# Performance work log

Measured on AMD Instinct MI355X. Metric: run time of the kernel, lower is better.

Reference implementation:

```python
import jax, jax.numpy as jnp
import numpy as np

NUM_HEADS = 8

def setup_inputs() -> dict:
    key = jax.random.key(0)
    k1, k2, k3, k4 = jax.random.split(key, 4)
    B, N, C = 2, 4096, 768
    x = jax.random.normal(k1, (B, N, C), dtype=jnp.float32)
    w_qkv = jax.random.normal(k2, (C, 3 * C), dtype=jnp.float32) * (C ** -0.5)
    w_proj = jax.random.normal(k3, (C, C), dtype=jnp.float32) * (C ** -0.5)
    b_proj = jax.random.normal(k4, (C,), dtype=jnp.float32) * 0.02
    return {"x": x, "w_qkv": w_qkv, "w_proj": w_proj, "b_proj": b_proj}

def reference(x, w_qkv, w_proj, b_proj):
    B, N, C = x.shape
    H = NUM_HEADS
    Dh = C // H
    scale = Dh ** -0.5
    # qkv: [B, N, 3C] -> [B, N, 3, H, Dh] -> [3, B, H, N, Dh]
    qkv = (x @ w_qkv).reshape(B, N, 3, H, Dh).transpose(2, 0, 3, 1, 4)
    q, k, v = qkv[0], qkv[1], qkv[2]
    attn = jnp.einsum('bhqd,bhkd->bhqk', q, k) * scale  # [B,H,N,N]
    attn = jax.nn.softmax(attn, axis=-1)
    out = jnp.einsum('bhqk,bhkd->bhqd', attn, v)        # [B,H,N,Dh]
    out = out.transpose(0, 2, 1, 3).reshape(B, N, C)
    return out @ w_proj + b_proj
```

## Files before the change

### kernel.cpp

```cpp
#include <hip/hip_runtime.h>
#include <hip/hip_bf16.h>

typedef __attribute__((ext_vector_type(8))) short short8;
typedef __attribute__((ext_vector_type(4))) short short4v;
typedef __attribute__((ext_vector_type(4))) float f32x4;
typedef __attribute__((ext_vector_type(16))) float f32x16;

#define MFMA16(a,b,c) __builtin_amdgcn_mfma_f32_16x16x32_bf16(a,b,c,0,0,0)
#define MFMA32(a,b,c) __builtin_amdgcn_mfma_f32_32x32x16_bf16(a,b,c,0,0,0)

__device__ __forceinline__ unsigned short f2b_rne(float f){
  union { float f; unsigned int u; } v; v.f = f;
  unsigned int u = v.u;
  return (unsigned short)((u + 0x7FFFu + ((u >> 16) & 1u)) >> 16);
}

__device__ __forceinline__ f32x16 zero16(){
  f32x16 z;
  #pragma unroll
  for (int i = 0; i < 16; ++i) z[i] = 0.f;
  return z;
}

__global__ __launch_bounds__(256) void k_cvt(const float* __restrict__ in,
                                             unsigned short* __restrict__ out, int n8){
  int i = blockIdx.x * 256 + threadIdx.x;
  if (i >= n8) return;
  const float4* p = (const float4*)in + (size_t)i * 2;
  float4 a = p[0], b = p[1];
  short8 o;
  o[0] = (short)f2b_rne(a.x); o[1] = (short)f2b_rne(a.y);
  o[2] = (short)f2b_rne(a.z); o[3] = (short)f2b_rne(a.w);
  o[4] = (short)f2b_rne(b.x); o[5] = (short)f2b_rne(b.y);
  o[6] = (short)f2b_rne(b.z); o[7] = (short)f2b_rne(b.w);
  *((short8*)out + i) = o;
}

__global__ void k_transpose_cvt(const float* __restrict__ in, unsigned short* __restrict__ out,
                                int R, int Cc){
  __shared__ unsigned short tile[32][33];
  int c0 = blockIdx.x * 32, r0 = blockIdx.y * 32;
  int tx = threadIdx.x, ty = threadIdx.y;
  #pragma unroll
  for (int i = 0; i < 32; i += 8)
    tile[ty + i][tx] = f2b_rne(in[(size_t)(r0 + ty + i) * Cc + c0 + tx]);
  __syncthreads();
  #pragma unroll
  for (int i = 0; i < 32; i += 8)
    out[(size_t)(c0 + ty + i) * R + r0 + tx] = tile[tx][ty + i];
}

__global__ __launch_bounds__(256) void k_gemm_qkv(
    const unsigned short* __restrict__ A,
    const unsigned short* __restrict__ Bt,
    unsigned short* __restrict__ qbuf,
    unsigned short* __restrict__ kbuf,
    unsigned short* __restrict__ vtb)
{
  __shared__ short As[128 * 40];
  __shared__ short Bs[128 * 40];
  int m0 = blockIdx.x * 128, n0 = blockIdx.y * 128;
  int t = threadIdx.x, l = t & 63, w = t >> 6;
  int lr = l & 15, lh = l >> 4;
  int wr = w >> 1, wc = w & 1;

  int row0 = t >> 2, cs0 = t & 3;
  int row1 = row0 + 64;
  const unsigned short* ga0 = A  + (size_t)(m0 + row0) * 768 + cs0 * 8;
  const unsigned short* ga1 = A  + (size_t)(m0 + row1) * 768 + cs0 * 8;
  const unsigned short* gb0 = Bt + (size_t)(n0 + row0) * 768 + cs0 * 8;
  const unsigned short* gb1 = Bt + (size_t)(n0 + row1) * 768 + cs0 * 8;
  short* la0 = As + row0 * 40 + cs0 * 8;
  short* la1 = As + row1 * 40 + cs0 * 8;
  short* lb0 = Bs + row0 * 40 + cs0 * 8;
  short* lb1 = Bs + row1 * 40 + cs0 * 8;

  f32x4 acc[4][4];
  f32x4 z4 = {0.f, 0.f, 0.f, 0.f};
  #pragma unroll
  for (int mf = 0; mf < 4; ++mf)
    #pragma unroll
    for (int nf = 0; nf < 4; ++nf) acc[mf][nf] = z4;

  short8 ra0 = *(const short8*)ga0;
  short8 ra1 = *(const short8*)ga1;
  short8 rb0 = *(const short8*)gb0;
  short8 rb1 = *(const short8*)gb1;

  for (int kt = 0; kt < 24; ++kt){
    __syncthreads();
    *(short8*)la0 = ra0; *(short8*)la1 = ra1;
    *(short8*)lb0 = rb0; *(short8*)lb1 = rb1;
    __syncthreads();
    if (kt < 23){
      ra0 = *(const short8*)(ga0 + (kt + 1) * 32);
      ra1 = *(const short8*)(ga1 + (kt + 1) * 32);
      rb0 = *(const short8*)(gb0 + (kt + 1) * 32);
      rb1 = *(const short8*)(gb1 + (kt + 1) * 32);
    }
    short8 af[4], bfm[4];
    #pragma unroll
    for (int mf = 0; mf < 4; ++mf)
      af[mf] = *(const short8*)(As + (wr * 64 + mf * 16 + lr) * 40 + lh * 8);
    #pragma unroll
    for (int nf = 0; nf < 4; ++nf)
      bfm[nf] = *(const short8*)(Bs + (wc * 64 + nf * 16 + lr) * 40 + lh * 8);
    #pragma unroll
    for (int mf = 0; mf < 4; ++mf)
      #pragma unroll
      for (int nf = 0; nf < 4; ++nf)
        acc[mf][nf] = MFMA16(af[mf], bfm[nf], acc[mf][nf]);
  }

  const float qscale = 0.10206207261596577f * 1.4426950408889634f;
  int three = n0 / 768;
  int b_ = m0 >> 12;
  int ntok0 = m0 & 4095;
  #pragma unroll
  for (int nf = 0; nf < 4; ++nf){
    int gcol = n0 + wc * 64 + nf * 16 + lr;
    int jj = gcol - three * 768;
    int h = jj / 96;
    int dh = jj - h * 96;
    #pragma unroll
    for (int mf = 0; mf < 4; ++mf){
      int ntok = ntok0 + wr * 64 + mf * 16 + lh * 4;
      if (three == 0){
        unsigned short* dst = qbuf + (size_t)(b_ * 8 + h) * 4096 * 96;
        #pragma unroll
        for (int r = 0; r < 4; ++r)
          dst[(size_t)(ntok + r) * 96 + dh] = f2b_rne(acc[mf][nf][r] * qscale);
      } else if (three == 1){
        unsigned short* dst = kbuf + (size_t)(b_ * 8 + h) * 4096 * 96;
        #pragma unroll
        for (int r = 0; r < 4; ++r)
          dst[(size_t)(ntok + r) * 96 + dh] = f2b_rne(acc[mf][nf][r]);
      } else {
        short4v sv;
        #pragma unroll
        for (int r = 0; r < 4; ++r) sv[r] = (short)f2b_rne(acc[mf][nf][r]);
        *(short4v*)(vtb + ((size_t)(b_ * 8 + h) * 96 + dh) * 4096 + ntok) = sv;
      }
    }
  }
}

__global__ __launch_bounds__(512) void k_attn2(
    const unsigned short* __restrict__ qb,
    const unsigned short* __restrict__ kb,
    const unsigned short* __restrict__ vtb,
    unsigned short* __restrict__ ao)
{
  __shared__ short lds[27136];
  const int bh = blockIdx.x;
  const int qt = blockIdx.y;
  const int tid = threadIdx.x;
  const int ln = tid & 63, wid = tid >> 6;
  const int qc = ln & 31, hi = ln >> 5;
  const int q0 = qt * 256 + wid * 32;

  const unsigned short* qbase = qb  + (size_t)bh * 4096 * 96;
  const unsigned short* kbase = kb  + (size_t)bh * 4096 * 96;
  const unsigned short* vbase = vtb + (size_t)bh * 96 * 4096;

  short8 qf[6];
  #pragma unroll
  for (int kw = 0; kw < 6; ++kw)
    qf[kw] = *(const short8*)(qbase + (size_t)(q0 + qc) * 96 + kw * 16 + hi * 8);

  const unsigned short* gp[3]; int gstep[3], loff[3], lstep[3];
  #pragma unroll
  for (int j = 0; j < 3; ++j){
    int c = tid + j * 512;
    if (c < 768){
      int r = c / 12, cl = c - r * 12;
      gp[j] = kbase + r * 96 + cl * 8; gstep[j] = 64 * 96;
      loff[j] = r * 104 + cl * 8;      lstep[j] = 6656;
    } else {
      int cv = c - 768; int r = cv >> 3, cl = cv & 7;
      gp[j] = vbase + (size_t)r * 4096 + cl * 8; gstep[j] = 64;
      loff[j] = 13312 + r * 72 + cl * 8;         lstep[j] = 6912;
    }
  }

  short8 rs[3];
  #pragma unroll
  for (int j = 0; j < 3; ++j){ rs[j] = *(const short8*)gp[j]; gp[j] += gstep[j]; }
  #pragma unroll
  for (int j = 0; j < 3; ++j) *(short8*)(lds + loff[j]) = rs[j];

  f32x16 oacc[3];
  #pragma unroll
  for (int dt = 0; dt < 3; ++dt) oacc[dt] = zero16();
  float m = -1e30f, lsum = 0.f;

  const int krd = qc * 104 + hi * 8;
  const int vrd = 13312 + qc * 72 + hi * 8;

#define CVTPK(d, lo_, hi_) asm("v_cvt_pk_bf16_f32 %0, %1, %2" : "=v"(d) : "v"(lo_), "v"(hi_))
#define PLSWAP(x_, y_)     asm("v_permlane32_swap_b32 %0, %1" : "+v"(x_), "+v"(y_))

  for (int kt = 0; kt < 64; ++kt){
    const int cur = kt & 1;
    __syncthreads();
    if (kt < 63){
      #pragma unroll
      for (int j = 0; j < 3; ++j){ rs[j] = *(const short8*)gp[j]; gp[j] += gstep[j]; }
    }
    const short* Kb = lds + cur * 6656 + krd;
    const short* Vb = lds + cur * 6912 + vrd;

    f32x16 s0 = zero16(), s1 = zero16();
    __builtin_amdgcn_s_setprio(1);
    #pragma unroll
    for (int kw = 0; kw < 6; ++kw){
      short8 kf = *(const short8*)(Kb + kw * 16);
      s0 = MFMA32(kf, qf[kw], s0);
    }
    #pragma unroll
    for (int kw = 0; kw < 6; ++kw){
      short8 kf = *(const short8*)(Kb + 32 * 104 + kw * 16);
      s1 = MFMA32(kf, qf[kw], s1);
    }
    __builtin_amdgcn_s_setprio(0);

    float tmax = s0[0];
    #pragma unroll
    for (int r = 1; r < 16; ++r) tmax = fmaxf(tmax, s0[r]);
    #pragma unroll
    for (int r = 0; r < 16; ++r) tmax = fmaxf(tmax, s1[r]);
    tmax = fmaxf(tmax, __shfl_xor(tmax, 32, 64));
    float mnew = fmaxf(m, tmax);
    float alpha = exp2f(m - mnew);
    m = mnew;
    float psum = 0.f;
    #pragma unroll
    for (int r = 0; r < 16; ++r){ float p = exp2f(s0[r] - m); s0[r] = p; psum += p; }
    #pragma unroll
    for (int r = 0; r < 16; ++r){ float p = exp2f(s1[r] - m); s1[r] = p; psum += p; }
    psum += __shfl_xor(psum, 32, 64);
    lsum = lsum * alpha + psum;
    #pragma unroll
    for (int dt = 0; dt < 3; ++dt)
      #pragma unroll
      for (int r = 0; r < 16; ++r) oacc[dt][r] *= alpha;

    short8 pa[4];
    {
      unsigned int a, b;
      union { unsigned int u[4]; short8 s; } pk;
      CVTPK(a, s0[0], s0[1]);  CVTPK(b, s0[4],  s0[5]);  PLSWAP(a, b); pk.u[0] = a; pk.u[2] = b;
      CVTPK(a, s0[2], s0[3]);  CVTPK(b, s0[6],  s0[7]);  PLSWAP(a, b); pk.u[1] = a; pk.u[3] = b;
      pa[0] = pk.s;
      CVTPK(a, s0[8], s0[9]);  CVTPK(b, s0[12], s0[13]); PLSWAP(a, b); pk.u[0] = a; pk.u[2] = b;
      CVTPK(a, s0[10], s0[11]); CVTPK(b, s0[14], s0[15]); PLSWAP(a, b); pk.u[1] = a; pk.u[3] = b;
      pa[1] = pk.s;
      CVTPK(a, s1[0], s1[1]);  CVTPK(b, s1[4],  s1[5]);  PLSWAP(a, b); pk.u[0] = a; pk.u[2] = b;
      CVTPK(a, s1[2], s1[3]);  CVTPK(b, s1[6],  s1[7]);  PLSWAP(a, b); pk.u[1] = a; pk.u[3] = b;
      pa[2] = pk.s;
      CVTPK(a, s1[8], s1[9]);  CVTPK(b, s1[12], s1[13]); PLSWAP(a, b); pk.u[0] = a; pk.u[2] = b;
      CVTPK(a, s1[10], s1[11]); CVTPK(b, s1[14], s1[15]); PLSWAP(a, b); pk.u[1] = a; pk.u[3] = b;
      pa[3] = pk.s;
    }

    __builtin_amdgcn_s_setprio(1);
    #pragma unroll
    for (int dt = 0; dt < 3; ++dt){
      #pragma unroll
      for (int w = 0; w < 4; ++w){
        short8 vf = *(const short8*)(Vb + dt * 32 * 72 + w * 16);
        oacc[dt] = MFMA32(vf, pa[w], oacc[dt]);
      }
    }
    __builtin_amdgcn_s_setprio(0);

    if (kt < 63){
      const int nb = cur ^ 1;
      #pragma unroll
      for (int j = 0; j < 3; ++j) *(short8*)(lds + loff[j] + nb * lstep[j]) = rs[j];
    }
  }

  float inv = 1.0f / lsum;
  int b_ = bh >> 3, h = bh & 7;
  unsigned short* orow = ao + (size_t)(b_ * 4096 + q0 + qc) * 768 + h * 96;
  #pragma unroll
  for (int dt = 0; dt < 3; ++dt)
    #pragma unroll
    for (int g = 0; g < 4; ++g){
      short4v sv;
      #pragma unroll
      for (int r = 0; r < 4; ++r) sv[r] = (short)f2b_rne(oacc[dt][g * 4 + r] * inv);
      *(short4v*)(orow + dt * 32 + g * 8 + hi * 4) = sv;
    }
#undef CVTPK
#undef PLSWAP
}

__global__ __launch_bounds__(256) void k_gemm_proj(
    const unsigned short* __restrict__ A,
    const unsigned short* __restrict__ Bt,
    const float* __restrict__ bias,
    float* __restrict__ out)
{
  __shared__ short As[128 * 40];
  __shared__ short Bs[128 * 40];
  int m0 = blockIdx.x * 128, n0 = blockIdx.y * 128;
  int t = threadIdx.x, l = t & 63, w = t >> 6;
  int lr = l & 15, lh = l >> 4;
  int wr = w >> 1, wc = w & 1;

  int row0 = t >> 2, cs0 = t & 3;
  int row1 = row0 + 64;
  const unsigned short* ga0 = A  + (size_t)(m0 + row0) * 768 + cs0 * 8;
  const unsigned short* ga1 = A  + (size_t)(m0 + row1) * 768 + cs0 * 8;
  const unsigned short* gb0 = Bt + (size_t)(n0 + row0) * 768 + cs0 * 8;
  const unsigned short* gb1 = Bt + (size_t)(n0 + row1) * 768 + cs0 * 8;
  short* la0 = As + row0 * 40 + cs0 * 8;
  short* la1 = As + row1 * 40 + cs0 * 8;
  short* lb0 = Bs + row0 * 40 + cs0 * 8;
  short* lb1 = Bs + row1 * 40 + cs0 * 8;

  f32x4 acc[4][4];
  f32x4 z4 = {0.f, 0.f, 0.f, 0.f};
  #pragma unroll
  for (int mf = 0; mf < 4; ++mf)
    #pragma unroll
    for (int nf = 0; nf < 4; ++nf) acc[mf][nf] = z4;

  short8 ra0 = *(const short8*)ga0;
  short8 ra1 = *(const short8*)ga1;
  short8 rb0 = *(const short8*)gb0;
  short8 rb1 = *(const short8*)gb1;

  for (int kt = 0; kt < 24; ++kt){
    __syncthreads();
    *(short8*)la0 = ra0; *(short8*)la1 = ra1;
    *(short8*)lb0 = rb0; *(short8*)lb1 = rb1;
    __syncthreads();
    if (kt < 23){
      ra0 = *(const short8*)(ga0 + (kt + 1) * 32);
      ra1 = *(const short8*)(ga1 + (kt + 1) * 32);
      rb0 = *(const short8*)(gb0 + (kt + 1) * 32);
      rb1 = *(const short8*)(gb1 + (kt + 1) * 32);
    }
    short8 af[4], bfm[4];
    #pragma unroll
    for (int mf = 0; mf < 4; ++mf)
      af[mf] = *(const short8*)(As + (wr * 64 + mf * 16 + lr) * 40 + lh * 8);
    #pragma unroll
    for (int nf = 0; nf < 4; ++nf)
      bfm[nf] = *(const short8*)(Bs + (wc * 64 + nf * 16 + lr) * 40 + lh * 8);
    #pragma unroll
    for (int mf = 0; mf < 4; ++mf)
      #pragma unroll
      for (int nf = 0; nf < 4; ++nf)
        acc[mf][nf] = MFMA16(af[mf], bfm[nf], acc[mf][nf]);
  }

  #pragma unroll
  for (int nf = 0; nf < 4; ++nf){
    int gcol = n0 + wc * 64 + nf * 16 + lr;
    float bb = bias[gcol];
    #pragma unroll
    for (int mf = 0; mf < 4; ++mf){
      int grow = m0 + wr * 64 + mf * 16 + lh * 4;
      #pragma unroll
      for (int r = 0; r < 4; ++r)
        out[(size_t)(grow + r) * 768 + gcol] = acc[mf][nf][r] + bb;
    }
  }
}

extern "C" void kernel_launch(void* const* d_in, const int* in_sizes, int n_in,
                              void* d_out, int out_size, void* d_ws, size_t ws_size,
                              hipStream_t stream) {
  const float* x      = (const float*)d_in[0];
  const float* w_qkv  = (const float*)d_in[1];
  const float* w_proj = (const float*)d_in[2];
  const float* b_proj = (const float*)d_in[3];
  float* out = (float*)d_out;
  char* ws = (char*)d_ws;

  unsigned short* xb     = (unsigned short*)(ws);
  unsigned short* wqkvt  = (unsigned short*)(ws + 12582912);
  unsigned short* wprojt = (unsigned short*)(ws + 16121856);
  unsigned short* qbuf   = (unsigned short*)(ws + 17301504);
  unsigned short* kbuf   = (unsigned short*)(ws + 29884416);
  unsigned short* vtb    = (unsigned short*)(ws + 42467328);
  unsigned short* aob    = xb;

  k_cvt<<<3072, 256, 0, stream>>>(x, xb, 786432);
  k_transpose_cvt<<<dim3(72, 24), dim3(32, 8), 0, stream>>>(w_qkv, wqkvt, 768, 2304);
  k_transpose_cvt<<<dim3(24, 24), dim3(32, 8), 0, stream>>>(w_proj, wprojt, 768, 768);
  k_gemm_qkv<<<dim3(64, 18), 256, 0, stream>>>(xb, wqkvt, qbuf, kbuf, vtb);
  k_attn2<<<dim3(16, 16), 512, 0, stream>>>(qbuf, kbuf, vtb, aob);
  k_gemm_proj<<<dim3(64, 6), 256, 0, stream>>>(aob, wprojt, b_proj, out);
}
```

Measured before the change: 229.5 us.

## Split KV range across two warp sets with 64-row queries per warp and lazy rescale

The attention kernel now has each warp handle 64 query rows (two 32-row groups), so every K/V fragment read from LDS feeds two MFMAs. The eight warps form two sets that process alternate 64-key tiles, and their partial softmax states are merged through LDS at the end. Online-softmax rescaling is skipped unless the running max grows by more than 8, and the global prefetch is placed between the two softmax passes. The cost is higher register pressure from doubled accumulators, a two-barrier single-buffer loop, and an LDS-based merge epilogue.

```diff
diff --git a/kernel.cpp b/kernel.cpp
--- a/kernel.cpp
+++ b/kernel.cpp
@@ -145,7 +145,7 @@
   }
 }
 
-__global__ __launch_bounds__(512) void k_attn2(
+__global__ __launch_bounds__(512) void k_attn3(
     const unsigned short* __restrict__ qb,
     const unsigned short* __restrict__ kb,
     const unsigned short* __restrict__ vtb,
@@ -157,144 +157,215 @@
   const int tid = threadIdx.x;
   const int ln = tid & 63, wid = tid >> 6;
   const int qc = ln & 31, hi = ln >> 5;
-  const int q0 = qt * 256 + wid * 32;
+  const int set = wid >> 2, qquad = wid & 3;
+  const int q0 = qt * 256 + qquad * 64;
 
   const unsigned short* qbase = qb  + (size_t)bh * 4096 * 96;
   const unsigned short* kbase = kb  + (size_t)bh * 4096 * 96;
   const unsigned short* vbase = vtb + (size_t)bh * 96 * 4096;
 
-  short8 qf[6];
-  #pragma unroll
-  for (int kw = 0; kw < 6; ++kw)
-    qf[kw] = *(const short8*)(qbase + (size_t)(q0 + qc) * 96 + kw * 16 + hi * 8);
-
-  const unsigned short* gp[3]; int gstep[3], loff[3], lstep[3];
-  #pragma unroll
-  for (int j = 0; j < 3; ++j){
+  short8 qf[2][6];
+  #pragma unroll
+  for (int g = 0; g < 2; ++g)
+    #pragma unroll
+    for (int kw = 0; kw < 6; ++kw)
+      qf[g][kw] = *(const short8*)(qbase + (size_t)(q0 + g * 32 + qc) * 96 + kw * 16 + hi * 8);
+
+  const unsigned short* gp[6]; int gstep[6], loff[6];
+  #pragma unroll
+  for (int j = 0; j < 6; ++j){
     int c = tid + j * 512;
-    if (c < 768){
-      int r = c / 12, cl = c - r * 12;
-      gp[j] = kbase + r * 96 + cl * 8; gstep[j] = 64 * 96;
-      loff[j] = r * 104 + cl * 8;      lstep[j] = 6656;
+    int s = (c >= 1536) ? 1 : 0;
+    int cc = c - s * 1536;
+    if (cc < 768){
+      int r = cc / 12, cl = cc - r * 12;
+      gp[j] = kbase + (size_t)(s * 64 + r) * 96 + cl * 8; gstep[j] = 12288;
+      loff[j] = s * 6656 + r * 104 + cl * 8;
     } else {
-      int cv = c - 768; int r = cv >> 3, cl = cv & 7;
-      gp[j] = vbase + (size_t)r * 4096 + cl * 8; gstep[j] = 64;
-      loff[j] = 13312 + r * 72 + cl * 8;         lstep[j] = 6912;
-    }
-  }
-
-  short8 rs[3];
-  #pragma unroll
-  for (int j = 0; j < 3; ++j){ rs[j] = *(const short8*)gp[j]; gp[j] += gstep[j]; }
-  #pragma unroll
-  for (int j = 0; j < 3; ++j) *(short8*)(lds + loff[j]) = rs[j];
-
-  f32x16 oacc[3];
-  #pragma unroll
-  for (int dt = 0; dt < 3; ++dt) oacc[dt] = zero16();
-  float m = -1e30f, lsum = 0.f;
-
-  const int krd = qc * 104 + hi * 8;
-  const int vrd = 13312 + qc * 72 + hi * 8;
+      int cv = cc - 768; int r = cv >> 3, cl = cv & 7;
+      gp[j] = vbase + (size_t)r * 4096 + s * 64 + cl * 8; gstep[j] = 128;
+      loff[j] = 13312 + s * 6912 + r * 72 + cl * 8;
+    }
+  }
+
+  short8 rs[6];
+  #pragma unroll
+  for (int j = 0; j < 6; ++j){ rs[j] = *(const short8*)gp[j]; gp[j] += gstep[j]; }
+  #pragma unroll
+  for (int j = 0; j < 6; ++j) *(short8*)(lds + loff[j]) = rs[j];
+
+  f32x16 oacc[2][3];
+  #pragma unroll
+  for (int g = 0; g < 2; ++g)
+    #pragma unroll
+    for (int dt = 0; dt < 3; ++dt) oacc[g][dt] = zero16();
+  float mr[2] = {-1e30f, -1e30f}, lr_[2] = {0.f, 0.f};
+
+  const short* Kb = lds + set * 6656 + qc * 104 + hi * 8;
+  const short* Vb = lds + 13312 + set * 6912 + qc * 72 + hi * 8;
 
 #define CVTPK(d, lo_, hi_) asm("v_cvt_pk_bf16_f32 %0, %1, %2" : "=v"(d) : "v"(lo_), "v"(hi_))
 #define PLSWAP(x_, y_)     asm("v_permlane32_swap_b32 %0, %1" : "+v"(x_), "+v"(y_))
 
-  for (int kt = 0; kt < 64; ++kt){
-    const int cur = kt & 1;
-    __syncthreads();
-    if (kt < 63){
-      #pragma unroll
-      for (int j = 0; j < 3; ++j){ rs[j] = *(const short8*)gp[j]; gp[j] += gstep[j]; }
-    }
-    const short* Kb = lds + cur * 6656 + krd;
-    const short* Vb = lds + cur * 6912 + vrd;
-
-    f32x16 s0 = zero16(), s1 = zero16();
+#define PA_BUILD(pa_, sA_, sB_)                                                          \
+  {                                                                                      \
+    unsigned int a_, b_;                                                                 \
+    union { unsigned int u[4]; short8 s; } pk_;                                          \
+    CVTPK(a_, sA_[0],  sA_[1]);  CVTPK(b_, sA_[4],  sA_[5]);  PLSWAP(a_, b_); pk_.u[0]=a_; pk_.u[2]=b_; \
+    CVTPK(a_, sA_[2],  sA_[3]);  CVTPK(b_, sA_[6],  sA_[7]);  PLSWAP(a_, b_); pk_.u[1]=a_; pk_.u[3]=b_; \
+    pa_[0] = pk_.s;                                                                      \
+    CVTPK(a_, sA_[8],  sA_[9]);  CVTPK(b_, sA_[12], sA_[13]); PLSWAP(a_, b_); pk_.u[0]=a_; pk_.u[2]=b_; \
+    CVTPK(a_, sA_[10], sA_[11]); CVTPK(b_, sA_[14], sA_[15]); PLSWAP(a_, b_); pk_.u[1]=a_; pk_.u[3]=b_; \
+    pa_[1] = pk_.s;                                                                      \
+    CVTPK(a_, sB_[0],  sB_[1]);  CVTPK(b_, sB_[4],  sB_[5]);  PLSWAP(a_, b_); pk_.u[0]=a_; pk_.u[2]=b_; \
+    CVTPK(a_, sB_[2],  sB_[3]);  CVTPK(b_, sB_[6],  sB_[7]);  PLSWAP(a_, b_); pk_.u[1]=a_; pk_.u[3]=b_; \
+    pa_[2] = pk_.s;                                                                      \
+    CVTPK(a_, sB_[8],  sB_[9]);  CVTPK(b_, sB_[12], sB_[13]); PLSWAP(a_, b_); pk_.u[0]=a_; pk_.u[2]=b_; \
+    CVTPK(a_, sB_[10], sB_[11]); CVTPK(b_, sB_[14], sB_[15]); PLSWAP(a_, b_); pk_.u[1]=a_; pk_.u[3]=b_; \
+    pa_[3] = pk_.s;                                                                      \
+  }
+
+#define SOFTMAX(g_, sA_, sB_)                                                            \
+  {                                                                                      \
+    float t0 = fmaxf(sA_[0], sA_[1]), t1 = fmaxf(sA_[2], sA_[3]);                        \
+    float t2 = fmaxf(sA_[4], sA_[5]), t3 = fmaxf(sA_[6], sA_[7]);                        \
+    t0 = fmaxf(t0, fmaxf(sA_[8],  sA_[9]));  t1 = fmaxf(t1, fmaxf(sA_[10], sA_[11]));    \
+    t2 = fmaxf(t2, fmaxf(sA_[12], sA_[13])); t3 = fmaxf(t3, fmaxf(sA_[14], sA_[15]));    \
+    t0 = fmaxf(t0, fmaxf(sB_[0],  sB_[1]));  t1 = fmaxf(t1, fmaxf(sB_[2],  sB_[3]));     \
+    t2 = fmaxf(t2, fmaxf(sB_[4],  sB_[5]));  t3 = fmaxf(t3, fmaxf(sB_[6],  sB_[7]));     \
+    t0 = fmaxf(t0, fmaxf(sB_[8],  sB_[9]));  t1 = fmaxf(t1, fmaxf(sB_[10], sB_[11]));    \
+    t2 = fmaxf(t2, fmaxf(sB_[12], sB_[13])); t3 = fmaxf(t3, fmaxf(sB_[14], sB_[15]));    \
+    float tmax = fmaxf(fmaxf(t0, t1), fmaxf(t2, t3));                                    \
+    tmax = fmaxf(tmax, __shfl_xor(tmax, 32, 64));                                        \
+    if (!__all(tmax - mr[g_] <= 8.0f)){                                                  \
+      float mn = fmaxf(mr[g_], tmax);                                                    \
+      float al = exp2f(mr[g_] - mn);                                                     \
+      _Pragma("unroll")                                                                  \
+      for (int dt = 0; dt < 3; ++dt)                                                     \
+        _Pragma("unroll")                                                                 \
+        for (int r = 0; r < 16; ++r) oacc[g_][dt][r] *= al;                              \
+      lr_[g_] *= al; mr[g_] = mn;                                                        \
+    }                                                                                    \
+    float p0 = 0.f, p1 = 0.f, p2 = 0.f, p3 = 0.f;                                        \
+    _Pragma("unroll")                                                                    \
+    for (int r = 0; r < 16; r += 4){                                                     \
+      sA_[r]   = exp2f(sA_[r]   - mr[g_]); p0 += sA_[r];                                 \
+      sA_[r+1] = exp2f(sA_[r+1] - mr[g_]); p1 += sA_[r+1];                               \
+      sA_[r+2] = exp2f(sA_[r+2] - mr[g_]); p2 += sA_[r+2];                               \
+      sA_[r+3] = exp2f(sA_[r+3] - mr[g_]); p3 += sA_[r+3];                               \
+    }                                                                                    \
+    _Pragma("unroll")                                                                    \
+    for (int r = 0; r < 16; r += 4){                                                     \
+      sB_[r]   = exp2f(sB_[r]   - mr[g_]); p0 += sB_[r];                                 \
+      sB_[r+1] = exp2f(sB_[r+1] - mr[g_]); p1 += sB_[r+1];                               \
+      sB_[r+2] = exp2f(sB_[r+2] - mr[g_]); p2 += sB_[r+2];                               \
+      sB_[r+3] = exp2f(sB_[r+3] - mr[g_]); p3 += sB_[r+3];                               \
+    }                                                                                    \
+    float psum = (p0 + p1) + (p2 + p3);                                                  \
+    psum += __shfl_xor(psum, 32, 64);                                                    \
+    lr_[g_] += psum;                                                                     \
+  }
+
+  for (int ss = 0; ss < 32; ++ss){
+    __syncthreads();
+
+    f32x16 s00 = zero16(), s01 = zero16(), s10 = zero16(), s11 = zero16();
     __builtin_amdgcn_s_setprio(1);
     #pragma unroll
     for (int kw = 0; kw < 6; ++kw){
       short8 kf = *(const short8*)(Kb + kw * 16);
-      s0 = MFMA32(kf, qf[kw], s0);
+      s00 = MFMA32(kf, qf[0][kw], s00);
+      s01 = MFMA32(kf, qf[1][kw], s01);
     }
     #pragma unroll
     for (int kw = 0; kw < 6; ++kw){
-      short8 kf = *(const short8*)(Kb + 32 * 104 + kw * 16);
-      s1 = MFMA32(kf, qf[kw], s1);
+      short8 kf = *(const short8*)(Kb + 3328 + kw * 16);
+      s10 = MFMA32(kf, qf[0][kw], s10);
+      s11 = MFMA32(kf, qf[1][kw], s11);
     }
     __builtin_amdgcn_s_setprio(0);
 
-    float tmax = s0[0];
-    #pragma unroll
-    for (int r = 1; r < 16; ++r) tmax = fmaxf(tmax, s0[r]);
-    #pragma unroll
-    for (int r = 0; r < 16; ++r) tmax = fmaxf(tmax, s1[r]);
-    tmax = fmaxf(tmax, __shfl_xor(tmax, 32, 64));
-    float mnew = fmaxf(m, tmax);
-    float alpha = exp2f(m - mnew);
-    m = mnew;
-    float psum = 0.f;
-    #pragma unroll
-    for (int r = 0; r < 16; ++r){ float p = exp2f(s0[r] - m); s0[r] = p; psum += p; }
-    #pragma unroll
-    for (int r = 0; r < 16; ++r){ float p = exp2f(s1[r] - m); s1[r] = p; psum += p; }
-    psum += __shfl_xor(psum, 32, 64);
-    lsum = lsum * alpha + psum;
-    #pragma unroll
-    for (int dt = 0; dt < 3; ++dt)
-      #pragma unroll
-      for (int r = 0; r < 16; ++r) oacc[dt][r] *= alpha;
-
-    short8 pa[4];
-    {
-      unsigned int a, b;
-      union { unsigned int u[4]; short8 s; } pk;
-      CVTPK(a, s0[0], s0[1]);  CVTPK(b, s0[4],  s0[5]);  PLSWAP(a, b); pk.u[0] = a; pk.u[2] = b;
-      CVTPK(a, s0[2], s0[3]);  CVTPK(b, s0[6],  s0[7]);  PLSWAP(a, b); pk.u[1] = a; pk.u[3] = b;
-      pa[0] = pk.s;
-      CVTPK(a, s0[8], s0[9]);  CVTPK(b, s0[12], s0[13]); PLSWAP(a, b); pk.u[0] = a; pk.u[2] = b;
-      CVTPK(a, s0[10], s0[11]); CVTPK(b, s0[14], s0[15]); PLSWAP(a, b); pk.u[1] = a; pk.u[3] = b;
-      pa[1] = pk.s;
-      CVTPK(a, s1[0], s1[1]);  CVTPK(b, s1[4],  s1[5]);  PLSWAP(a, b); pk.u[0] = a; pk.u[2] = b;
-      CVTPK(a, s1[2], s1[3]);  CVTPK(b, s1[6],  s1[7]);  PLSWAP(a, b); pk.u[1] = a; pk.u[3] = b;
-      pa[2] = pk.s;
-      CVTPK(a, s1[8], s1[9]);  CVTPK(b, s1[12], s1[13]); PLSWAP(a, b); pk.u[0] = a; pk.u[2] = b;
-      CVTPK(a, s1[10], s1[11]); CVTPK(b, s1[14], s1[15]); PLSWAP(a, b); pk.u[1] = a; pk.u[3] = b;
-      pa[3] = pk.s;
-    }
+    SOFTMAX(0, s00, s10)
+    short8 pa0[4];
+    PA_BUILD(pa0, s00, s10)
+
+    if (ss < 31){
+      #pragma unroll
+      for (int j = 0; j < 6; ++j){ rs[j] = *(const short8*)gp[j]; gp[j] += gstep[j]; }
+    }
+
+    SOFTMAX(1, s01, s11)
+    short8 pa1[4];
+    PA_BUILD(pa1, s01, s11)
 
     __builtin_amdgcn_s_setprio(1);
     #pragma unroll
     for (int dt = 0; dt < 3; ++dt){
       #pragma unroll
       for (int w = 0; w < 4; ++w){
-        short8 vf = *(const short8*)(Vb + dt * 32 * 72 + w * 16);
-        oacc[dt] = MFMA32(vf, pa[w], oacc[dt]);
+        short8 vf = *(const short8*)(Vb + dt * 2304 + w * 16);
+        oacc[0][dt] = MFMA32(vf, pa0[w], oacc[0][dt]);
+        oacc[1][dt] = MFMA32(vf, pa1[w], oacc[1][dt]);
       }
     }
     __builtin_amdgcn_s_setprio(0);
 
-    if (kt < 63){
-      const int nb = cur ^ 1;
-      #pragma unroll
-      for (int j = 0; j < 3; ++j) *(short8*)(lds + loff[j] + nb * lstep[j]) = rs[j];
-    }
-  }
-
-  float inv = 1.0f / lsum;
-  int b_ = bh >> 3, h = bh & 7;
-  unsigned short* orow = ao + (size_t)(b_ * 4096 + q0 + qc) * 768 + h * 96;
-  #pragma unroll
-  for (int dt = 0; dt < 3; ++dt)
-    #pragma unroll
-    for (int g = 0; g < 4; ++g){
-      short4v sv;
-      #pragma unroll
-      for (int r = 0; r < 4; ++r) sv[r] = (short)f2b_rne(oacc[dt][g * 4 + r] * inv);
-      *(short4v*)(orow + dt * 32 + g * 8 + hi * 4) = sv;
-    }
+    __syncthreads();
+    if (ss < 31){
+      #pragma unroll
+      for (int j = 0; j < 6; ++j) *(short8*)(lds + loff[j]) = rs[j];
+    }
+  }
+
+  float* fl = (float*)lds;
+  #pragma unroll
+  for (int g = 0; g < 2; ++g){
+    __syncthreads();
+    if (set == 1){
+      #pragma unroll
+      for (int dt = 0; dt < 3; ++dt)
+        #pragma unroll
+        for (int r = 0; r < 16; ++r)
+          fl[qquad * 3072 + dt * 1024 + r * 64 + ln] = oacc[g][dt][r];
+      fl[12288 + qquad * 64 + ln] = mr[g];
+      fl[12544 + qquad * 64 + ln] = lr_[g];
+    }
+    __syncthreads();
+    if (set == 0){
+      float m1v = fl[12288 + qquad * 64 + ln];
+      float l1v = fl[12544 + qquad * 64 + ln];
+      float M  = fmaxf(mr[g], m1v);
+      float w0 = exp2f(mr[g] - M), w1 = exp2f(m1v - M);
+      lr_[g] = w0 * lr_[g] + w1 * l1v;
+      #pragma unroll
+      for (int dt = 0; dt < 3; ++dt)
+        #pragma unroll
+        for (int r = 0; r < 16; ++r)
+          oacc[g][dt][r] = w0 * oacc[g][dt][r] + w1 * fl[qquad * 3072 + dt * 1024 + r * 64 + ln];
+    }
+  }
+
+  if (set == 0){
+    int b_ = bh >> 3, h = bh & 7;
+    #pragma unroll
+    for (int g = 0; g < 2; ++g){
+      float inv = 1.0f / lr_[g];
+      unsigned short* orow = ao + (size_t)(b_ * 4096 + q0 + g * 32 + qc) * 768 + h * 96;
+      #pragma unroll
+      for (int dt = 0; dt < 3; ++dt)
+        #pragma unroll
+        for (int g4 = 0; g4 < 4; ++g4){
+          short4v sv;
+          #pragma unroll
+          for (int r = 0; r < 4; ++r) sv[r] = (short)f2b_rne(oacc[g][dt][g4 * 4 + r] * inv);
+          *(short4v*)(orow + dt * 32 + g4 * 8 + hi * 4) = sv;
+        }
+    }
+  }
 #undef CVTPK
 #undef PLSWAP
+#undef PA_BUILD
+#undef SOFTMAX
 }
 
 __global__ __launch_bounds__(256) void k_gemm_proj(
@@ -394,6 +465,6 @@
   k_transpose_cvt<<<dim3(72, 24), dim3(32, 8), 0, stream>>>(w_qkv, wqkvt, 768, 2304);
   k_transpose_cvt<<<dim3(24, 24), dim3(32, 8), 0, stream>>>(w_proj, wprojt, 768, 768);
   k_gemm_qkv<<<dim3(64, 18), 256, 0, stream>>>(xb, wqkvt, qbuf, kbuf, vtb);
-  k_attn2<<<dim3(16, 16), 512, 0, stream>>>(qbuf, kbuf, vtb, aob);
+  k_attn3<<<dim3(16, 16), 512, 0, stream>>>(qbuf, kbuf, vtb, aob);
   k_gemm_proj<<<dim3(64, 6), 256, 0, stream>>>(aob, wprojt, b_proj, out);
 }
```

Result: slower. 288.0 us (+25.5%).
